# Kernel optimization log

Hardware: AMD Instinct MI355X
Metric: run time of the kernel (lower is better)

Reference implementation:

```python
import jax, jax.numpy as jnp
import numpy as np

B, T, C, H = 2, 2048, 1024, 16
HD = C // H  # head dim = 64


def setup_inputs() -> dict:
    key = jax.random.key(0)
    k0, k1, k2 = jax.random.split(key, 3)
    x = jax.random.normal(k0, (B, T, C), jnp.float32)
    W_attn = jax.random.normal(k1, (C, 3 * C), jnp.float32) * 0.02
    b_attn = jnp.zeros((3 * C,), jnp.float32)
    W_proj = jax.random.normal(k2, (C, C), jnp.float32) * 0.02
    b_proj = jnp.zeros((C,), jnp.float32)
    # rope: (1,1,T,HD//2,2,2) stack of 2x2 rotation matrices [[cos,-sin],[sin,cos]]
    inv_freq = 1.0 / (10000.0 ** (jnp.arange(0, HD, 2, dtype=jnp.float32) / HD))
    ang = jnp.arange(T, dtype=jnp.float32)[:, None] * inv_freq[None, :]  # (T, HD//2)
    cos, sin = jnp.cos(ang), jnp.sin(ang)
    rope = jnp.stack([jnp.stack([cos, -sin], -1), jnp.stack([sin, cos], -1)], -2)
    rope = rope[None, None]  # (1,1,T,HD//2,2,2)
    return dict(x=x, W_attn=W_attn, b_attn=b_attn, W_proj=W_proj, b_proj=b_proj, rope=rope)


def reference(x, W_attn, b_attn, W_proj, b_proj, rope):
    Bv, Tv, Cv = x.shape
    Hd = Cv // H
    qkv = x @ W_attn + b_attn                      # (B,T,3C) fused QKV proj
    q, k, v = jnp.split(qkv, 3, axis=-1)

    def heads(t):
        return t.reshape(Bv, Tv, H, Hd).transpose(0, 2, 1, 3)  # (B,H,T,Hd)

    q, k, v = heads(q), heads(k), heads(v)

    cos = rope[..., 0, 0][..., None]               # (1,1,T,Hd//2,1)
    sin = rope[..., 1, 0][..., None]

    def rot(t):
        tr = t.reshape(Bv, H, Tv, Hd // 2, 2)
        xr, yr = tr[..., 0:1], tr[..., 1:2]
        out = jnp.concatenate([xr * cos - yr * sin, xr * sin + yr * cos], axis=-1)
        return out.reshape(Bv, H, Tv, Hd)

    q, k = rot(q), rot(k)

    scale = 1.0 / np.sqrt(Hd).astype(np.float32)
    att = jnp.einsum('bhqd,bhkd->bhqk', q, k) * scale
    mask = jnp.tril(jnp.ones((Tv, Tv), dtype=bool))  # causal
    att = jnp.where(mask[None, None], att, -jnp.inf)
    att = jax.nn.softmax(att, axis=-1)
    y = jnp.einsum('bhqk,bhkd->bhqd', att, v)
    y = y.transpose(0, 2, 1, 3).reshape(Bv, Tv, Cv)
    return y @ W_proj + b_proj
```

## Files before the change

### kernel.cpp

```cpp
#include <hip/hip_runtime.h>
#include <hip/hip_bf16.h>

typedef __attribute__((ext_vector_type(8))) short short8;
typedef __attribute__((ext_vector_type(4))) short short4b;
typedef __attribute__((ext_vector_type(4))) float f32x4;
typedef __attribute__((ext_vector_type(16))) float f32x16;
typedef __attribute__((ext_vector_type(4))) unsigned u32x4;

static constexpr int Bb = 2, Tt = 2048, Cc = 1024, Hh = 16;
static constexpr int BT = Bb * Tt;
static constexpr int N1 = 3 * Cc;
static constexpr float QS = 0.125f * 1.44269504f;

__device__ __forceinline__ unsigned short f2b(float f) {
  union { float f; unsigned u; } v; v.f = f;
  unsigned r = v.u + 0x7fffu + ((v.u >> 16) & 1u);
  return (unsigned short)(r >> 16);
}
__device__ __forceinline__ float b2f(short s) {
  union { unsigned u; float f; } v; v.u = ((unsigned)(unsigned short)s) << 16;
  return v.f;
}

__global__ __launch_bounds__(256) void k_cast(const float* __restrict__ in,
                                              unsigned short* __restrict__ out, int n) {
  int i = (blockIdx.x * 256 + threadIdx.x) * 8;
  if (i >= n) return;
  float4 a = *reinterpret_cast<const float4*>(in + i);
  float4 b = *reinterpret_cast<const float4*>(in + i + 4);
  short8 o;
  o[0] = f2b(a.x); o[1] = f2b(a.y); o[2] = f2b(a.z); o[3] = f2b(a.w);
  o[4] = f2b(b.x); o[5] = f2b(b.y); o[6] = f2b(b.z); o[7] = f2b(b.w);
  *reinterpret_cast<short8*>(out + i) = o;
}

__global__ __launch_bounds__(256) void k_tcast(const float* __restrict__ in,
                                               unsigned short* __restrict__ out,
                                               int R, int Ccol) {
  __shared__ float tile[32][33];
  int cb = blockIdx.x * 32, rb = blockIdx.y * 32;
  int tx = threadIdx.x & 31, ty = threadIdx.x >> 5;
  for (int i = 0; i < 32; i += 8)
    tile[ty + i][tx] = in[(size_t)(rb + ty + i) * Ccol + cb + tx];
  __syncthreads();
  for (int i = 0; i < 32; i += 8)
    out[(size_t)(cb + ty + i) * R + rb + tx] = f2b(tile[tx][ty + i]);
}

template <int NF, int EPI>
__global__ __launch_bounds__(512, 2)
void k_gemm8(const unsigned short* __restrict__ A, const unsigned short* __restrict__ Bt,
             const float* __restrict__ bias, void* __restrict__ Cout,
             const float* __restrict__ rope, unsigned short* __restrict__ Qs,
             unsigned short* __restrict__ Ks, unsigned short* __restrict__ Vt,
             int M, int N, int K) {
  constexpr int BN = NF * 64;
  constexpr int ASZ = 256 * 64;
  constexpr int BSZ = BN * 64;
  constexpr int STRIDE = ASZ + BSZ;
  extern __shared__ unsigned short lds[];
  const int tid = threadIdx.x, lane = tid & 63, w = tid >> 6;
  const int wm = w >> 2, wn = w & 3;
  const int l15 = lane & 15, l4 = lane >> 4;
  int nbx = gridDim.x;
  int lin = blockIdx.y * nbx + blockIdx.x;
  int cpx = (nbx * gridDim.y) >> 3;
  lin = (lin & 7) * cpx + (lin >> 3);
  const int mb = lin / nbx, nb = lin % nbx;
  const size_t arow0 = (size_t)mb * 256;
  const size_t brow0 = (size_t)nb * BN;

  const int srow = lane >> 3;
  const int scol = (((lane & 7) * 16) ^ (srow << 4)) >> 1;
  auto stage = [&](int buf, int k0) {
    unsigned short* Ab = lds + buf * STRIDE;
    unsigned short* Bb = Ab + ASZ;
#pragma unroll
    for (int i = 0; i < 4; i++) {
      int c = w + 8 * i;
      const unsigned short* g = A + (arow0 + c * 8 + srow) * (size_t)K + k0 + scol;
      __builtin_amdgcn_global_load_lds((const __attribute__((address_space(1))) void*)g,
          (__attribute__((address_space(3))) void*)(Ab + c * 512), 16, 0, 0);
    }
#pragma unroll
    for (int i = 0; i < NF; i++) {
      int c = w + 8 * i;
      const unsigned short* g = Bt + (brow0 + c * 8 + srow) * (size_t)K + k0 + scol;
      __builtin_amdgcn_global_load_lds((const __attribute__((address_space(1))) void*)g,
          (__attribute__((address_space(3))) void*)(Bb + c * 512), 16, 0, 0);
    }
  };

  f32x4 acc[8][NF] = {};
  const int NK = K >> 6;

  stage(0, 0);
  asm volatile("s_waitcnt vmcnt(0)" ::: "memory");
  asm volatile("s_barrier" ::: "memory");

  for (int kt = 0; kt < NK; kt++) {
    int buf = kt & 1;
    if (kt + 1 < NK) stage(buf ^ 1, (kt + 1) << 6);
    const unsigned short* Ab = lds + buf * STRIDE;
    const unsigned short* Bb = Ab + ASZ;
    short8 af[8][2];
#pragma unroll
    for (int p = 0; p < NF; p++) {
      if (p == 0) {
#pragma unroll
        for (int m = 0; m < 8; m++) {
          int ra = wm * 128 + m * 16 + l15;
#pragma unroll
          for (int kk = 0; kk < 2; kk++) {
            int cb = (kk * 64 + l4 * 16) ^ ((ra & 7) << 4);
            af[m][kk] = *reinterpret_cast<const short8*>(Ab + ra * 64 + (cb >> 1));
          }
        }
      }
      short8 bfr[2];
      int rb = wn * (NF * 16) + p * 16 + l15;
#pragma unroll
      for (int kk = 0; kk < 2; kk++) {
        int cb = (kk * 64 + l4 * 16) ^ ((rb & 7) << 4);
        bfr[kk] = *reinterpret_cast<const short8*>(Bb + rb * 64 + (cb >> 1));
      }
      asm volatile("s_barrier" ::: "memory");
      asm volatile("s_waitcnt lgkmcnt(0)" ::: "memory");
      __builtin_amdgcn_sched_barrier(0);
      __builtin_amdgcn_s_setprio(1);
#pragma unroll
      for (int m = 0; m < 8; m++) {
        acc[m][p] = __builtin_amdgcn_mfma_f32_16x16x32_bf16(af[m][0], bfr[0], acc[m][p], 0, 0, 0);
        acc[m][p] = __builtin_amdgcn_mfma_f32_16x16x32_bf16(af[m][1], bfr[1], acc[m][p], 0, 0, 0);
      }
      __builtin_amdgcn_s_setprio(0);
      if (p == NF - 1)
        asm volatile("s_waitcnt vmcnt(0)" ::: "memory");
      asm volatile("s_barrier" ::: "memory");
    }
  }

#pragma unroll
  for (int m = 0; m < 8; m++) {
#pragma unroll
    for (int n = 0; n < NF; n++) {
      int ccol0 = nb * BN + wn * (NF * 16) + n * 16;
      float bv = bias[ccol0 + l15];
      int r0 = mb * 256 + wm * 128 + m * 16 + l4 * 4;
      if (EPI == 0) {
#pragma unroll
        for (int j = 0; j < 4; j++)
          ((float*)Cout)[(size_t)(r0 + j) * N + ccol0 + l15] = acc[m][n][j] + bv;
      } else {
        int cls = ccol0 >> 10;
        int h = (ccol0 >> 6) & 15;
        int d = (ccol0 & 63) + l15;
        int bq = r0 >> 11;
        int t0 = r0 & 2047;
        size_t bh = (size_t)bq * 16 + h;
        if (cls == 2) {
          short4b o;
#pragma unroll
          for (int j = 0; j < 4; j++) o[j] = (short)f2b(acc[m][n][j] + bv);
          *reinterpret_cast<short4b*>(Vt + (bh * 64 + d) * Tt + t0) = o;
        } else {
          unsigned short* dst = (cls == 0) ? Qs : Ks;
          int jj = d >> 1;
          int odd = d & 1;
#pragma unroll
          for (int j = 0; j < 4; j++) {
            float v = acc[m][n][j] + bv;
            float part = __shfl_xor(v, 1);
            float2 sc = *reinterpret_cast<const float2*>(
                rope + (size_t)(t0 + j) * 128 + jj * 4 + 2);
            float x = odd ? part : v;
            float y = odd ? v : part;
            float rot = odd ? (x * sc.x + y * sc.y)
                            : (x * sc.y - y * sc.x);
            if (cls == 0) rot *= QS;
            dst[(bh * Tt + (t0 + j)) * 64 + d] = f2b(rot);
          }
        }
      }
    }
  }
}

__device__ __forceinline__ float tmax16(const f32x16& v) {
  float a0 = fmaxf(v[0], v[1]),   a1 = fmaxf(v[2], v[3]);
  float a2 = fmaxf(v[4], v[5]),   a3 = fmaxf(v[6], v[7]);
  float a4 = fmaxf(v[8], v[9]),   a5 = fmaxf(v[10], v[11]);
  float a6 = fmaxf(v[12], v[13]), a7 = fmaxf(v[14], v[15]);
  float b0 = fmaxf(a0, a1), b1 = fmaxf(a2, a3), b2 = fmaxf(a4, a5), b3 = fmaxf(a6, a7);
  return fmaxf(fmaxf(b0, b1), fmaxf(b2, b3));
}

template <bool DIAG>
__device__ __forceinline__ void attn_tile128(
    const unsigned short* Kl, const unsigned short* Vl,
    int w, int l31, int hi, const short8 qf[4],
    float& m_run, float& l_run, f32x16 oacc[2]) {
  const int ktmax = DIAG ? w : 3;
  f32x16 s[4];
#pragma unroll
  for (int kt = 0; kt < 4; kt++) {
    if (kt > ktmax) continue;
    f32x16 acc = {};
    int rk = kt * 32 + l31;
    int sw = (rk & 7) << 4;
    const unsigned short* krow = Kl + rk * 64;
#pragma unroll
    for (int kk = 0; kk < 4; kk++) {
      short8 kf = *reinterpret_cast<const short8*>(krow + (((kk * 32 + hi * 16) ^ sw) >> 1));
      acc = __builtin_amdgcn_mfma_f32_32x32x16_bf16(kf, qf[kk], acc, 0, 0, 0);
    }
    if (DIAG && kt == w) {
#pragma unroll
      for (int r = 0; r < 16; r++) {
        int e = (r & 3) + 8 * (r >> 2) + 4 * hi;
        if (e > l31) acc[r] = -1e30f;
      }
    }
    s[kt] = acc;
  }
  float km[4];
#pragma unroll
  for (int kt = 0; kt < 4; kt++) km[kt] = (kt <= ktmax) ? tmax16(s[kt]) : -1e30f;
  float mx = fmaxf(fmaxf(km[0], km[1]), fmaxf(km[2], km[3]));
  mx = fmaxf(mx, __shfl_xor(mx, 32));
  float nm = fmaxf(m_run, mx);
  float fsc = __builtin_amdgcn_exp2f(m_run - nm);
  m_run = nm;
#pragma unroll
  for (int dt = 0; dt < 2; dt++)
#pragma unroll
    for (int r = 0; r < 16; r++) oacc[dt][r] *= fsc;

  float kps[4] = {0.f, 0.f, 0.f, 0.f};
#pragma unroll
  for (int kt = 0; kt < 4; kt++) {
    if (kt > ktmax) continue;
    float p[16];
#pragma unroll
    for (int r = 0; r < 16; r++) p[r] = __builtin_amdgcn_exp2f(s[kt][r] - nm);
    float s0 = (p[0] + p[1]) + (p[2] + p[3]);
    float s1 = (p[4] + p[5]) + (p[6] + p[7]);
    float s2 = (p[8] + p[9]) + (p[10] + p[11]);
    float s3 = (p[12] + p[13]) + (p[14] + p[15]);
    kps[kt] = (s0 + s1) + (s2 + s3);
    unsigned P[8];
#pragma unroll
    for (int i = 0; i < 8; i++) {
      unsigned lo = (__builtin_bit_cast(unsigned, p[2 * i]) + 0x8000u) >> 16;
      unsigned h2 = (__builtin_bit_cast(unsigned, p[2 * i + 1]) + 0x8000u) & 0xffff0000u;
      P[i] = lo | h2;
    }
    unsigned Y0 = (unsigned)__shfl_xor((int)(hi ? P[0] : P[2]), 32);
    unsigned Y1 = (unsigned)__shfl_xor((int)(hi ? P[1] : P[3]), 32);
    unsigned Y2 = (unsigned)__shfl_xor((int)(hi ? P[4] : P[6]), 32);
    unsigned Y3 = (unsigned)__shfl_xor((int)(hi ? P[5] : P[7]), 32);
    u32x4 c0 = hi ? u32x4{Y0, Y1, P[2], P[3]} : u32x4{P[0], P[1], Y0, Y1};
    u32x4 c1 = hi ? u32x4{Y2, Y3, P[6], P[7]} : u32x4{P[4], P[5], Y2, Y3};
    short8 pf0 = __builtin_bit_cast(short8, c0);
    short8 pf1 = __builtin_bit_cast(short8, c1);
#pragma unroll
    for (int dt = 0; dt < 2; dt++) {
      int d = dt * 32 + l31;
      int sv = (d & 15) << 4;
      const unsigned short* vrow = Vl + d * 128;
      short8 vf0 = *reinterpret_cast<const short8*>(vrow + (((kt * 64 + hi * 16) ^ sv) >> 1));
      short8 vf1 = *reinterpret_cast<const short8*>(vrow + (((kt * 64 + 32 + hi * 16) ^ sv) >> 1));
      oacc[dt] = __builtin_amdgcn_mfma_f32_32x32x16_bf16(vf0, pf0, oacc[dt], 0, 0, 0);
      oacc[dt] = __builtin_amdgcn_mfma_f32_32x32x16_bf16(vf1, pf1, oacc[dt], 0, 0, 0);
    }
  }
  float psum = (kps[0] + kps[1]) + (kps[2] + kps[3]);
  psum += __shfl_xor(psum, 32);
  l_run = l_run * fsc + psum;
}

__global__ __launch_bounds__(256)
void k_attn(const unsigned short* __restrict__ Qs, const unsigned short* __restrict__ Ks,
            const unsigned short* __restrict__ Vt, unsigned short* __restrict__ Y) {
  __shared__ unsigned short lds[32768];
  int tid = threadIdx.x, lane = tid & 63, w = tid >> 6;
  int s = blockIdx.x;
  int xcd = s & 7;
  int o = s >> 3;
  int bh = xcd * 4 + (o & 3);
  int qb = (o < 32) ? (15 - (o >> 2)) : ((o - 32) >> 2);
  int b = bh >> 4, h = bh & 15;
  int l31 = lane & 31, hi = lane >> 5;
  int qw0 = qb * 128 + w * 32;
  const unsigned short* Qb = Qs + (size_t)bh * Tt * 64;
  const unsigned short* Kb = Ks + (size_t)bh * Tt * 64;
  const unsigned short* Vb = Vt + (size_t)bh * 64 * Tt;

  auto stage = [&](int buf, int kv0) {
    unsigned short* Kbuf = lds + buf * 8192;
    unsigned short* Vbuf = lds + 16384 + buf * 8192;
    int krow = lane >> 3;
    int kcolb = ((lane & 7) * 16) ^ ((krow & 7) << 4);
#pragma unroll
    for (int cc = 0; cc < 4; cc++) {
      int c = w + cc * 4;
      const unsigned short* gk = Kb + (size_t)(kv0 + c * 8 + krow) * 64 + (kcolb >> 1);
      __builtin_amdgcn_global_load_lds((const __attribute__((address_space(1))) void*)gk,
          (__attribute__((address_space(3))) void*)(Kbuf + c * 512), 16, 0, 0);
      int vr = c * 4 + (lane >> 4);
      int vcolb = ((lane & 15) * 16) ^ ((vr & 15) << 4);
      const unsigned short* gv = Vb + (size_t)vr * Tt + kv0 + (vcolb >> 1);
      __builtin_amdgcn_global_load_lds((const __attribute__((address_space(1))) void*)gv,
          (__attribute__((address_space(3))) void*)(Vbuf + c * 512), 16, 0, 0);
    }
  };

  short8 qf[4];
#pragma unroll
  for (int kk = 0; kk < 4; kk++)
    qf[kk] = *reinterpret_cast<const short8*>(Qb + (size_t)(qw0 + l31) * 64 + kk * 16 + hi * 8);

  float m_run = -1e30f, l_run = 0.f;
  f32x16 oacc[2] = {};
  const int nt = qb + 1;

  stage(0, 0);
  __syncthreads();
  int cur = 0;
  for (int it = 0; it < nt - 1; ++it) {
    stage(cur ^ 1, (it + 1) * 128);
    attn_tile128<false>(lds + cur * 8192, lds + 16384 + cur * 8192,
                        w, l31, hi, qf, m_run, l_run, oacc);
    __syncthreads();
    cur ^= 1;
  }
  attn_tile128<true>(lds + cur * 8192, lds + 16384 + cur * 8192,
                     w, l31, hi, qf, m_run, l_run, oacc);

  float inv = 1.0f / l_run;
  int t = qw0 + l31;
  unsigned short* yrow = Y + ((size_t)b * Tt + t) * Cc + h * 64;
#pragma unroll
  for (int dt = 0; dt < 2; dt++)
#pragma unroll
    for (int q4 = 0; q4 < 4; q4++) {
      short4b oo;
#pragma unroll
      for (int jj = 0; jj < 4; jj++) oo[jj] = (short)f2b(oacc[dt][q4 * 4 + jj] * inv);
      *reinterpret_cast<short4b*>(yrow + dt * 32 + q4 * 8 + hi * 4) = oo;
    }
}

extern "C" void kernel_launch(void* const* d_in, const int* in_sizes, int n_in,
                              void* d_out, int out_size, void* d_ws, size_t ws_size,
                              hipStream_t stream) {
  (void)in_sizes; (void)n_in; (void)out_size; (void)ws_size;
  const float* x      = (const float*)d_in[0];
  const float* W_attn = (const float*)d_in[1];
  const float* b_attn = (const float*)d_in[2];
  const float* W_proj = (const float*)d_in[3];
  const float* b_proj = (const float*)d_in[4];
  const float* rope   = (const float*)d_in[5];
  float* out = (float*)d_out;

  char* ws = (char*)d_ws;
  unsigned short* xb  = (unsigned short*)(ws);
  unsigned short* WaT = (unsigned short*)(ws + (8u << 20));
  unsigned short* WpT = (unsigned short*)(ws + (14u << 20));
  unsigned short* Qs  = (unsigned short*)(ws + (16u << 20));
  unsigned short* Ks  = (unsigned short*)(ws + (24u << 20));
  unsigned short* Vt  = (unsigned short*)(ws + (32u << 20));
  unsigned short* Yb  = (unsigned short*)(ws + (40u << 20));

  constexpr int LDS_QKV  = (256 + 192) * 64 * 2 * 2;
  constexpr int LDS_PROJ = (256 + 128) * 64 * 2 * 2;
  (void)hipFuncSetAttribute(reinterpret_cast<const void*>(&k_gemm8<3, 1>),
                            hipFuncAttributeMaxDynamicSharedMemorySize, LDS_QKV);
  (void)hipFuncSetAttribute(reinterpret_cast<const void*>(&k_gemm8<2, 0>),
                            hipFuncAttributeMaxDynamicSharedMemorySize, LDS_PROJ);

  k_cast<<<2048, 256, 0, stream>>>(x, xb, BT * Cc);
  k_tcast<<<dim3(N1 / 32, Cc / 32), 256, 0, stream>>>(W_attn, WaT, Cc, N1);
  k_tcast<<<dim3(Cc / 32, Cc / 32), 256, 0, stream>>>(W_proj, WpT, Cc, Cc);
  k_gemm8<3, 1><<<dim3(N1 / 192, BT / 256), 512, LDS_QKV, stream>>>(
      xb, WaT, b_attn, nullptr, rope, Qs, Ks, Vt, BT, N1, Cc);
  k_attn<<<Bb * Hh * (Tt / 128), 256, 0, stream>>>(Qs, Ks, Vt, Yb);
  k_gemm8<2, 0><<<dim3(Cc / 128, BT / 256), 512, LDS_PROJ, stream>>>(
      Yb, WpT, b_proj, out, nullptr, nullptr, nullptr, nullptr, BT, Cc, Cc);
}
```

Before: 128.6 us.

## Add lazy softmax rescale, packed bf16 convert, MFMA priority and new block mapping

In the attention inner tile, the online-softmax rescale of the accumulator is skipped unless some lane's new max exceeds the running max by more than a threshold (wave-uniform via __all). The manual bf16 rounding of P is replaced with the v_cvt_pk_bf16_f32 instruction. K fragment loads are hoisted ahead of the MFMA chain, and MFMA groups are wrapped in s_setprio to favour matrix issue. The block-to-(bh,qb) mapping is also changed from an XCD-aware interleave to a simple half/pair split. Lazy rescaling trades exactness of the max for fewer multiplies and may allow exponent values above 1. The remapping may hurt L2 locality across XCDs.

```diff
diff --git a/kernel.cpp b/kernel.cpp
--- a/kernel.cpp
+++ b/kernel.cpp
@@ -209,11 +209,15 @@
     int rk = kt * 32 + l31;
     int sw = (rk & 7) << 4;
     const unsigned short* krow = Kl + rk * 64;
-#pragma unroll
-    for (int kk = 0; kk < 4; kk++) {
-      short8 kf = *reinterpret_cast<const short8*>(krow + (((kk * 32 + hi * 16) ^ sw) >> 1));
-      acc = __builtin_amdgcn_mfma_f32_32x32x16_bf16(kf, qf[kk], acc, 0, 0, 0);
-    }
+    short8 kf[4];
+#pragma unroll
+    for (int kk = 0; kk < 4; kk++)
+      kf[kk] = *reinterpret_cast<const short8*>(krow + (((kk * 32 + hi * 16) ^ sw) >> 1));
+    __builtin_amdgcn_s_setprio(1);
+#pragma unroll
+    for (int kk = 0; kk < 4; kk++)
+      acc = __builtin_amdgcn_mfma_f32_32x32x16_bf16(kf[kk], qf[kk], acc, 0, 0, 0);
+    __builtin_amdgcn_s_setprio(0);
     if (DIAG && kt == w) {
 #pragma unroll
       for (int r = 0; r < 16; r++) {
@@ -228,13 +232,17 @@
   for (int kt = 0; kt < 4; kt++) km[kt] = (kt <= ktmax) ? tmax16(s[kt]) : -1e30f;
   float mx = fmaxf(fmaxf(km[0], km[1]), fmaxf(km[2], km[3]));
   mx = fmaxf(mx, __shfl_xor(mx, 32));
-  float nm = fmaxf(m_run, mx);
-  float fsc = __builtin_amdgcn_exp2f(m_run - nm);
-  m_run = nm;
-#pragma unroll
-  for (int dt = 0; dt < 2; dt++)
-#pragma unroll
-    for (int r = 0; r < 16; r++) oacc[dt][r] *= fsc;
+
+  float fsc = 1.f;
+  if (!__all(mx <= m_run + 8.f)) {
+    float nm = fmaxf(m_run, mx);
+    fsc = __builtin_amdgcn_exp2f(m_run - nm);
+    m_run = nm;
+#pragma unroll
+    for (int dt = 0; dt < 2; dt++)
+#pragma unroll
+      for (int r = 0; r < 16; r++) oacc[dt][r] *= fsc;
+  }
 
   float kps[4] = {0.f, 0.f, 0.f, 0.f};
 #pragma unroll
@@ -242,7 +250,7 @@
     if (kt > ktmax) continue;
     float p[16];
 #pragma unroll
-    for (int r = 0; r < 16; r++) p[r] = __builtin_amdgcn_exp2f(s[kt][r] - nm);
+    for (int r = 0; r < 16; r++) p[r] = __builtin_amdgcn_exp2f(s[kt][r] - m_run);
     float s0 = (p[0] + p[1]) + (p[2] + p[3]);
     float s1 = (p[4] + p[5]) + (p[6] + p[7]);
     float s2 = (p[8] + p[9]) + (p[10] + p[11]);
@@ -250,11 +258,8 @@
     kps[kt] = (s0 + s1) + (s2 + s3);
     unsigned P[8];
 #pragma unroll
-    for (int i = 0; i < 8; i++) {
-      unsigned lo = (__builtin_bit_cast(unsigned, p[2 * i]) + 0x8000u) >> 16;
-      unsigned h2 = (__builtin_bit_cast(unsigned, p[2 * i + 1]) + 0x8000u) & 0xffff0000u;
-      P[i] = lo | h2;
-    }
+    for (int i = 0; i < 8; i++)
+      asm("v_cvt_pk_bf16_f32 %0, %1, %2" : "=v"(P[i]) : "v"(p[2 * i]), "v"(p[2 * i + 1]));
     unsigned Y0 = (unsigned)__shfl_xor((int)(hi ? P[0] : P[2]), 32);
     unsigned Y1 = (unsigned)__shfl_xor((int)(hi ? P[1] : P[3]), 32);
     unsigned Y2 = (unsigned)__shfl_xor((int)(hi ? P[4] : P[6]), 32);
@@ -270,8 +275,10 @@
       const unsigned short* vrow = Vl + d * 128;
       short8 vf0 = *reinterpret_cast<const short8*>(vrow + (((kt * 64 + hi * 16) ^ sv) >> 1));
       short8 vf1 = *reinterpret_cast<const short8*>(vrow + (((kt * 64 + 32 + hi * 16) ^ sv) >> 1));
+      __builtin_amdgcn_s_setprio(1);
       oacc[dt] = __builtin_amdgcn_mfma_f32_32x32x16_bf16(vf0, pf0, oacc[dt], 0, 0, 0);
       oacc[dt] = __builtin_amdgcn_mfma_f32_32x32x16_bf16(vf1, pf1, oacc[dt], 0, 0, 0);
+      __builtin_amdgcn_s_setprio(0);
     }
   }
   float psum = (kps[0] + kps[1]) + (kps[2] + kps[3]);
@@ -285,10 +292,11 @@
   __shared__ unsigned short lds[32768];
   int tid = threadIdx.x, lane = tid & 63, w = tid >> 6;
   int s = blockIdx.x;
-  int xcd = s & 7;
-  int o = s >> 3;
-  int bh = xcd * 4 + (o & 3);
-  int qb = (o < 32) ? (15 - (o >> 2)) : ((o - 32) >> 2);
+  int half = s >> 8;
+  int p = s & 255;
+  int bh = p >> 3;
+  int j = p & 7;
+  int qb = half ? j : 15 - j;
   int b = bh >> 4, h = bh & 15;
   int l31 = lane & 31, hi = lane >> 5;
   int qw0 = qb * 128 + w * 32;
```

Result: faster. 121.6 us (-5.4%).
